# Optimization experiments

Measured on AMD Instinct MI355X. Metric: run time of the kernel, lower is better.

The kernel has to match this reference:

```python
import jax, jax.numpy as jnp
import numpy as np

FORGET_RADIX = 10
HIDDEN_RADIX = 23
LN2 = float(np.log(2.0))
MAX_FORGET = 0.875
BATCH, IN_SIZE, H_SIZE = 8192, 1024, 2048
G = H_SIZE // 2  # group size (h_size // 2)


def setup_inputs() -> dict:
    key = jax.random.key(0)
    ks = jax.random.split(key, 6)
    x = jax.random.normal(ks[0], (BATCH, IN_SIZE), dtype=jnp.float32)
    # hidden is a fixed-point (radix 23) int state; values correspond to floats in (-0.125, 0.125)
    hidden = jax.random.randint(ks[1], (BATCH, H_SIZE), -(2**20), 2**20, dtype=jnp.int32)

    def lin(k, fan_in, fan_out):
        kw, kb = jax.random.split(k)
        s = 1.0 / np.sqrt(fan_in)
        W = jax.random.uniform(kw, (fan_in, fan_out), jnp.float32, -s, s)
        b = jax.random.uniform(kb, (fan_out,), jnp.float32, -s, s)
        return W, b

    W_zr1, b_zr1 = lin(ks[2], IN_SIZE + G, H_SIZE)
    W_g1, b_g1 = lin(ks[3], IN_SIZE + G, G)
    W_zr2, b_zr2 = lin(ks[4], IN_SIZE + G, H_SIZE)
    W_g2, b_g2 = lin(ks[5], IN_SIZE + G, G)
    return {"x": x, "hidden": hidden,
            "W_zr1": W_zr1, "b_zr1": b_zr1, "W_g1": W_g1, "b_g1": b_g1,
            "W_zr2": W_zr2, "b_zr2": b_zr2, "W_g2": W_g2, "b_g2": b_g2,
            "slice_dim": 0}


def _to_float(h_fix, radix):
    # ConvertToFloat: fixed-point int -> float
    return h_fix.astype(jnp.float32) / np.float32(2.0 ** radix)


def _to_fixed(v, radix):
    # ConvertToFixed: float -> fixed-point int (truncation toward zero, like Tensor.int())
    return jnp.trunc(v * np.float32(2.0 ** radix)).astype(jnp.int64)


def reference(x, hidden, W_zr1, b_zr1, W_g1, b_g1, W_zr2, b_zr2, W_g2, b_g2, slice_dim):
    h = hidden.astype(jnp.int64)  # widen so h * z_fix (up to ~2^34) does not overflow
    h1, h2 = h[:, :G], h[:, G:]

    # ---- group 1 update (reads h2) ----
    h2_fl = _to_float(h2, HIDDEN_RADIX)
    zr1 = jax.nn.sigmoid(jnp.concatenate([x, h2_fl], axis=1) @ W_zr1 + b_zr1)
    z1, r1 = zr1[:, :G], zr1[:, G:]
    z1 = MAX_FORGET * z1 + (1.0 - MAX_FORGET)
    g1 = jnp.tanh(jnp.concatenate([x, r1 * h2_fl], axis=1) @ W_g1 + b_g1)
    z1_fix = jnp.maximum(_to_fixed(z1, FORGET_RADIX), 1)  # EnsureNotForgetAll
    h1 = jnp.floor_divide(h1 * z1_fix, 2 ** FORGET_RADIX)  # FixedMultiply, buf=None, mask=1
    h1 = h1 + _to_fixed((1.0 - z1) * g1, HIDDEN_RADIX)     # + MaskFixedMultiply(update1, 1)

    # ---- group 2 update (reads updated h1) ----
    h1_fl = _to_float(h1, HIDDEN_RADIX)
    zr2 = jax.nn.sigmoid(jnp.concatenate([x, h1_fl], axis=1) @ W_zr2 + b_zr2)
    z2, r2 = zr2[:, :G], zr2[:, G:]
    z2 = MAX_FORGET * z2 + (1.0 - MAX_FORGET)
    g2 = jnp.tanh(jnp.concatenate([x, r2 * h1_fl], axis=1) @ W_g2 + b_g2)
    z2_fix = jnp.maximum(_to_fixed(z2, FORGET_RADIX), 1)
    h2 = jnp.floor_divide(h2 * z2_fix, 2 ** FORGET_RADIX)
    h2 = h2 + _to_fixed((1.0 - z2) * g2, HIDDEN_RADIX)

    recurrent_hidden = jnp.concatenate([h1, h2], axis=1).astype(jnp.int32)
    output_hidden = recurrent_hidden.astype(jnp.float32) / np.float32(2.0 ** HIDDEN_RADIX)

    optimal_bits = (jnp.sum(-jnp.log(z1[:, slice_dim:]) / LN2)
                    + jnp.sum(-jnp.log(z2) / LN2)
                    + 32.0 * slice_dim * x.shape[0])
    return recurrent_hidden, output_hidden, optimal_bits
```

## Files before the change

### kernel.cpp

```cpp
#include <hip/hip_runtime.h>
#include <hip/hip_bf16.h>

#define BATCH   8192
#define IN_SZ   1024
#define HSZ     2048
#define GG      1024
#define KTOT    2048

typedef __hip_bfloat16 bf16;
typedef __attribute__((ext_vector_type(8))) short  short8;
typedef __attribute__((ext_vector_type(4))) float  floatx4;

typedef __attribute__((address_space(1))) const void gvoid_t;
typedef __attribute__((address_space(3))) void       lvoid_t;

__device__ __forceinline__ void async_ld16(void* lds, const void* g) {
  __builtin_amdgcn_global_load_lds((gvoid_t*)g, (lvoid_t*)lds, 16, 0, 0);
}

__global__ void prep_kernel(const float* __restrict__ x, bf16* __restrict__ xb,
                            const int* __restrict__ hidden, bf16* __restrict__ hf,
                            float* accp) {
  int idx = blockIdx.x * blockDim.x + threadIdx.x;
  int i = idx * 4;
  float4 xv = *(const float4*)(x + i);
  xb[i + 0] = __float2bfloat16(xv.x);
  xb[i + 1] = __float2bfloat16(xv.y);
  xb[i + 2] = __float2bfloat16(xv.z);
  xb[i + 3] = __float2bfloat16(xv.w);
  int m = i >> 10, j = i & 1023;
  int4 hv = *(const int4*)(hidden + m * HSZ + GG + j);
  const float sc = 1.0f / 8388608.0f;
  hf[i + 0] = __float2bfloat16((float)hv.x * sc);
  hf[i + 1] = __float2bfloat16((float)hv.y * sc);
  hf[i + 2] = __float2bfloat16((float)hv.z * sc);
  hf[i + 3] = __float2bfloat16((float)hv.w * sc);
  if (idx == 0) *accp = 0.0f;
}

__global__ void transpose_cast(const float* __restrict__ W, bf16* __restrict__ Wt,
                               int K, int N) {
  __shared__ float tile[32][33];
  int bx = blockIdx.x, by = blockIdx.y;
  int tx = threadIdx.x, ty = threadIdx.y;
  int n_in = bx * 32 + tx;
  int k_in = by * 32 + ty;
#pragma unroll
  for (int s = 0; s < 32; s += 8)
    tile[ty + s][tx] = W[(size_t)(k_in + s) * N + n_in];
  __syncthreads();
  int n_out = bx * 32 + ty;
  int k_out = by * 32 + tx;
#pragma unroll
  for (int s = 0; s < 32; s += 8)
    Wt[(size_t)(n_out + s) * K + k_out] = __float2bfloat16(tile[tx][ty + s]);
}

__device__ __forceinline__ void gemm_mainloop(const bf16* __restrict__ Aleft,
                                              const bf16* __restrict__ Aright,
                                              const bf16* __restrict__ Bt,
                                              bf16* As, bf16* Bs,
                                              int m0, int n0, floatx4 acc[4][4]) {
  int t = threadIdx.x;
  int r = t >> 2, c = t & 3;
  int lane = t & 63;
  int q = lane >> 4, r16 = lane & 15;
  int w = t >> 6;
  int wm = w & 1, wn = w >> 1;

  const size_t arow0 = (size_t)(m0 + r) * IN_SZ;
  const size_t arow1 = (size_t)(m0 + r + 64) * IN_SZ;
  const size_t brow0 = (size_t)(n0 + r) * KTOT;
  const size_t brow1 = (size_t)(n0 + r + 64) * KTOT;
  bf16* lA0 = As + t * 8;
  bf16* lA1 = As + 64 * 32 + t * 8;
  bf16* lB0 = Bs + t * 8;
  bf16* lB1 = Bs + 64 * 32 + t * 8;
  const bf16* aRd = As + (wm * 64 + r16) * 32 + q * 8;
  const bf16* bRd = Bs + (wn * 64 + r16) * 32 + q * 8;

  for (int kb = 0; kb < KTOT / 32; ++kb) {
    int kt = kb * 32;
    const bf16* asrc; int kloc;
    if (kt < IN_SZ) { asrc = Aleft;  kloc = kt; }
    else            { asrc = Aright; kloc = kt - IN_SZ; }
    int ac = kloc + c * 8;
    async_ld16(lA0, asrc + arow0 + ac);
    async_ld16(lA1, asrc + arow1 + ac);
    int bc = kt + c * 8;
    async_ld16(lB0, Bt + brow0 + bc);
    async_ld16(lB1, Bt + brow1 + bc);
    __syncthreads();
    short8 af[4], bfr[4];
#pragma unroll
    for (int i = 0; i < 4; ++i) af[i]  = *(const short8*)(const void*)(aRd + i * 16 * 32);
#pragma unroll
    for (int j = 0; j < 4; ++j) bfr[j] = *(const short8*)(const void*)(bRd + j * 16 * 32);
#pragma unroll
    for (int i = 0; i < 4; ++i)
#pragma unroll
      for (int j = 0; j < 4; ++j)
        acc[i][j] = __builtin_amdgcn_mfma_f32_16x16x32_bf16(af[i], bfr[j], acc[i][j], 0, 0, 0);
    __syncthreads();
  }
}

__global__ void gemm_zr(const bf16* __restrict__ xb, const bf16* __restrict__ hfp,
                        const bf16* __restrict__ Bt, const float* __restrict__ bias,
                        float* __restrict__ zbuf, bf16* __restrict__ rh,
                        const int* __restrict__ slice_ptr, int use_slice,
                        float* __restrict__ accp) {
  __shared__ bf16 As[128 * 32];
  __shared__ bf16 Bs[128 * 32];
  floatx4 acc[4][4];
#pragma unroll
  for (int i = 0; i < 4; ++i)
#pragma unroll
    for (int j = 0; j < 4; ++j) acc[i][j] = (floatx4)0.0f;

  int m0 = blockIdx.y * 128, n0 = blockIdx.x * 128;
  gemm_mainloop(xb, hfp, Bt, As, Bs, m0, n0, acc);

  int t = threadIdx.x;
  int lane = t & 63, q = lane >> 4, r16 = lane & 15;
  int w = t >> 6, wm = w & 1, wn = w >> 1;
  int nmin = use_slice ? *slice_ptr : 0;
  float lsum = 0.0f;

#pragma unroll
  for (int i = 0; i < 4; ++i) {
    int mbase = m0 + wm * 64 + i * 16 + q * 4;
#pragma unroll
    for (int j = 0; j < 4; ++j) {
      int n = n0 + wn * 64 + j * 16 + r16;
      float bn = bias[n];
#pragma unroll
      for (int rr = 0; rr < 4; ++rr) {
        int m = mbase + rr;
        float v = acc[i][j][rr] + bn;
        float s = 1.0f / (1.0f + __expf(-v));
        if (n < GG) {
          float z = 0.875f * s + 0.125f;
          zbuf[(size_t)m * GG + n] = z;
          if (n >= nmin) lsum += -__log2f(z);
        } else {
          int jc = n - GG;
          float hfl = __bfloat162float(hfp[(size_t)m * GG + jc]);
          rh[(size_t)m * GG + jc] = __float2bfloat16(s * hfl);
        }
      }
    }
  }
  __syncthreads();
  float* sf = (float*)As;
#pragma unroll
  for (int off = 32; off > 0; off >>= 1) lsum += __shfl_down(lsum, off, 64);
  if (lane == 0) sf[w] = lsum;
  __syncthreads();
  if (t == 0) atomicAdd(accp, sf[0] + sf[1] + sf[2] + sf[3]);
}

__global__ void gemm_g(const bf16* __restrict__ xb, const bf16* __restrict__ rh,
                       const bf16* __restrict__ Bt, const float* __restrict__ bias,
                       const float* __restrict__ zbuf, const int* __restrict__ hidden,
                       int col_off,
                       float* __restrict__ out0, float* __restrict__ out1,
                       bf16* __restrict__ hf_out, int write_hf,
                       int write_bits, const float* __restrict__ accp,
                       const int* __restrict__ slice_ptr, float* __restrict__ out2) {
  __shared__ bf16 As[128 * 32];
  __shared__ bf16 Bs[128 * 32];
  floatx4 acc[4][4];
#pragma unroll
  for (int i = 0; i < 4; ++i)
#pragma unroll
    for (int j = 0; j < 4; ++j) acc[i][j] = (floatx4)0.0f;

  int m0 = blockIdx.y * 128, n0 = blockIdx.x * 128;
  gemm_mainloop(xb, rh, Bt, As, Bs, m0, n0, acc);

  int t = threadIdx.x;
  int lane = t & 63, q = lane >> 4, r16 = lane & 15;
  int w = t >> 6, wm = w & 1, wn = w >> 1;

#pragma unroll
  for (int i = 0; i < 4; ++i) {
    int mbase = m0 + wm * 64 + i * 16 + q * 4;
#pragma unroll
    for (int j = 0; j < 4; ++j) {
      int n = n0 + wn * 64 + j * 16 + r16;
      float bn = bias[n];
#pragma unroll
      for (int rr = 0; rr < 4; ++rr) {
        int m = mbase + rr;
        float v = acc[i][j][rr] + bn;
        float e = __expf(2.0f * v);
        float g = 1.0f - 2.0f / (e + 1.0f);
        float z = zbuf[(size_t)m * GG + n];
        int zfix = (int)(z * 1024.0f);
        if (zfix < 1) zfix = 1;
        long long h = hidden[(size_t)m * HSZ + col_off + n];
        long long hupd = (h * (long long)zfix) >> 10;
        float t2 = (1.0f - z) * g * 8388608.0f;
        long long f2 = (long long)t2;
        int hnew = (int)(hupd + f2);
        size_t oidx = (size_t)m * HSZ + col_off + n;
        out0[oidx] = (float)hnew;
        float ofl = (float)hnew * (1.0f / 8388608.0f);
        out1[oidx] = ofl;
        if (write_hf) hf_out[(size_t)m * GG + n] = __float2bfloat16(ofl);
      }
    }
  }
  if (write_bits && blockIdx.x == 0 && blockIdx.y == 0 && t == 0) {
    *out2 = *accp + 32.0f * (float)(*slice_ptr) * (float)BATCH;
  }
}

extern "C" void kernel_launch(void* const* d_in, const int* in_sizes, int n_in,
                              void* d_out, int out_size, void* d_ws, size_t ws_size,
                              hipStream_t stream) {
  const float* x      = (const float*)d_in[0];
  const int*   hidden = (const int*)d_in[1];
  const float* W_zr1  = (const float*)d_in[2];
  const float* b_zr1  = (const float*)d_in[3];
  const float* W_g1   = (const float*)d_in[4];
  const float* b_g1   = (const float*)d_in[5];
  const float* W_zr2  = (const float*)d_in[6];
  const float* b_zr2  = (const float*)d_in[7];
  const float* W_g2   = (const float*)d_in[8];
  const float* b_g2   = (const float*)d_in[9];
  const int*   slice  = (const int*)d_in[10];

  char* ws = (char*)d_ws;
  size_t off = 0;
  auto alloc = [&](size_t bytes) -> void* {
    void* p = ws + off;
    off += (bytes + 255) & ~(size_t)255;
    return p;
  };
  bf16* xb     = (bf16*)alloc((size_t)BATCH * IN_SZ * 2);
  bf16* wt_zr1 = (bf16*)alloc((size_t)2048 * 2048 * 2);
  bf16* wt_g1  = (bf16*)alloc((size_t)1024 * 2048 * 2);
  bf16* wt_zr2 = (bf16*)alloc((size_t)2048 * 2048 * 2);
  bf16* wt_g2  = (bf16*)alloc((size_t)1024 * 2048 * 2);
  bf16* hf     = (bf16*)alloc((size_t)BATCH * GG * 2);
  bf16* rh     = (bf16*)alloc((size_t)BATCH * GG * 2);
  float* zbuf  = (float*)alloc((size_t)BATCH * GG * 4);
  float* accp  = (float*)alloc(256);

  float* out0 = (float*)d_out;
  float* out1 = out0 + (size_t)BATCH * HSZ;
  float* out2 = out0 + 2 * (size_t)BATCH * HSZ;

  prep_kernel<<<BATCH * IN_SZ / 4 / 256, 256, 0, stream>>>(x, xb, hidden, hf, accp);
  transpose_cast<<<dim3(64, 64), dim3(32, 8), 0, stream>>>(W_zr1, wt_zr1, 2048, 2048);
  transpose_cast<<<dim3(32, 64), dim3(32, 8), 0, stream>>>(W_g1,  wt_g1,  2048, 1024);
  transpose_cast<<<dim3(64, 64), dim3(32, 8), 0, stream>>>(W_zr2, wt_zr2, 2048, 2048);
  transpose_cast<<<dim3(32, 64), dim3(32, 8), 0, stream>>>(W_g2,  wt_g2,  2048, 1024);

  gemm_zr<<<dim3(16, 64), 256, 0, stream>>>(xb, hf, wt_zr1, b_zr1, zbuf, rh, slice, 1, accp);
  gemm_g<<<dim3(8, 64), 256, 0, stream>>>(xb, rh, wt_g1, b_g1, zbuf, hidden, 0,
                                          out0, out1, hf, 1, 0, accp, slice, out2);
  gemm_zr<<<dim3(16, 64), 256, 0, stream>>>(xb, hf, wt_zr2, b_zr2, zbuf, rh, slice, 0, accp);
  gemm_g<<<dim3(8, 64), 256, 0, stream>>>(xb, rh, wt_g2, b_g2, zbuf, hidden, 1024,
                                          out0, out1, hf, 0, 1, accp, slice, out2);
}
```

Before: 658.6 us.

## Swizzle LDS tiles, halve gemm_g M-tile, store z as bf16, fuse prep kernels

Merges the input casting and four weight transposes into one launch, using a vectorized 64x64 transpose tile. XOR-swizzles the LDS chunk placement to reduce bank conflicts on MFMA operand reads. Halves the M tile of the gate GEMM to double its block count for better CU fill, and stores the forget gate buffer as bf16 to cut its memory traffic. The bf16 z buffer can shift the fixed-point forget value by a few units, which risks output mismatches.

```diff
diff --git a/kernel.cpp b/kernel.cpp
--- a/kernel.cpp
+++ b/kernel.cpp
@@ -18,55 +18,75 @@
   __builtin_amdgcn_global_load_lds((gvoid_t*)g, (lvoid_t*)lds, 16, 0, 0);
 }
 
-__global__ void prep_kernel(const float* __restrict__ x, bf16* __restrict__ xb,
-                            const int* __restrict__ hidden, bf16* __restrict__ hf,
-                            float* accp) {
-  int idx = blockIdx.x * blockDim.x + threadIdx.x;
-  int i = idx * 4;
-  float4 xv = *(const float4*)(x + i);
-  xb[i + 0] = __float2bfloat16(xv.x);
-  xb[i + 1] = __float2bfloat16(xv.y);
-  xb[i + 2] = __float2bfloat16(xv.z);
-  xb[i + 3] = __float2bfloat16(xv.w);
-  int m = i >> 10, j = i & 1023;
-  int4 hv = *(const int4*)(hidden + m * HSZ + GG + j);
-  const float sc = 1.0f / 8388608.0f;
-  hf[i + 0] = __float2bfloat16((float)hv.x * sc);
-  hf[i + 1] = __float2bfloat16((float)hv.y * sc);
-  hf[i + 2] = __float2bfloat16((float)hv.z * sc);
-  hf[i + 3] = __float2bfloat16((float)hv.w * sc);
-  if (idx == 0) *accp = 0.0f;
-}
-
-__global__ void transpose_cast(const float* __restrict__ W, bf16* __restrict__ Wt,
-                               int K, int N) {
-  __shared__ float tile[32][33];
-  int bx = blockIdx.x, by = blockIdx.y;
-  int tx = threadIdx.x, ty = threadIdx.y;
-  int n_in = bx * 32 + tx;
-  int k_in = by * 32 + ty;
-#pragma unroll
-  for (int s = 0; s < 32; s += 8)
-    tile[ty + s][tx] = W[(size_t)(k_in + s) * N + n_in];
-  __syncthreads();
-  int n_out = bx * 32 + ty;
-  int k_out = by * 32 + tx;
-#pragma unroll
-  for (int s = 0; s < 32; s += 8)
-    Wt[(size_t)(n_out + s) * K + k_out] = __float2bfloat16(tile[tx][ty + s]);
-}
-
+__global__ void prep_all(const float* __restrict__ x, bf16* __restrict__ xb,
+                         const int* __restrict__ hidden, bf16* __restrict__ hf,
+                         float* accp,
+                         const float* __restrict__ W_zr1, const float* __restrict__ W_g1,
+                         const float* __restrict__ W_zr2, const float* __restrict__ W_g2,
+                         bf16* __restrict__ wt_zr1, bf16* __restrict__ wt_g1,
+                         bf16* __restrict__ wt_zr2, bf16* __restrict__ wt_g2) {
+  int b = blockIdx.x;
+  int t = threadIdx.x;
+  if (b < 3072) {
+    const float* W; bf16* Wt; int N; int tb = b;
+    if (tb < 1024)      { W = W_zr1; Wt = wt_zr1; N = 2048; }
+    else if (tb < 1536) { W = W_g1;  Wt = wt_g1;  N = 1024; tb -= 1024; }
+    else if (tb < 2560) { W = W_zr2; Wt = wt_zr2; N = 2048; tb -= 1536; }
+    else                { W = W_g2;  Wt = wt_g2;  N = 1024; tb -= 2560; }
+    int ntn = N >> 6;
+    int k0 = (tb / ntn) * 64, n0 = (tb % ntn) * 64;
+    __shared__ float tile[64][65];
+    int kk = t >> 4, nn = (t & 15) * 4;
+#pragma unroll
+    for (int s = 0; s < 4; ++s) {
+      int row = kk + s * 16;
+      float4 v = *(const float4*)&W[(size_t)(k0 + row) * N + n0 + nn];
+      tile[row][nn + 0] = v.x; tile[row][nn + 1] = v.y;
+      tile[row][nn + 2] = v.z; tile[row][nn + 3] = v.w;
+    }
+    __syncthreads();
+    int k8 = (t & 7) * 8;
+#pragma unroll
+    for (int s = 0; s < 2; ++s) {
+      int nl = (t >> 3) + s * 32;
+      bf16 vals[8];
+#pragma unroll
+      for (int u = 0; u < 8; ++u) vals[u] = __float2bfloat16(tile[k8 + u][nl]);
+      *(short8*)&Wt[(size_t)(n0 + nl) * KTOT + k0 + k8] = *(short8*)vals;
+    }
+  } else {
+    int idx = (b - 3072) * 256 + t;
+    int i = idx * 4;
+    float4 xv = *(const float4*)(x + i);
+    xb[i + 0] = __float2bfloat16(xv.x);
+    xb[i + 1] = __float2bfloat16(xv.y);
+    xb[i + 2] = __float2bfloat16(xv.z);
+    xb[i + 3] = __float2bfloat16(xv.w);
+    int m = i >> 10, j = i & 1023;
+    int4 hv = *(const int4*)(hidden + m * HSZ + GG + j);
+    const float sc = 1.0f / 8388608.0f;
+    hf[i + 0] = __float2bfloat16((float)hv.x * sc);
+    hf[i + 1] = __float2bfloat16((float)hv.y * sc);
+    hf[i + 2] = __float2bfloat16((float)hv.z * sc);
+    hf[i + 3] = __float2bfloat16((float)hv.w * sc);
+    if (idx == 0) *accp = 0.0f;
+  }
+}
+
+template<int BM, int MI>
 __device__ __forceinline__ void gemm_mainloop(const bf16* __restrict__ Aleft,
                                               const bf16* __restrict__ Aright,
                                               const bf16* __restrict__ Bt,
                                               bf16* As, bf16* Bs,
-                                              int m0, int n0, floatx4 acc[4][4]) {
-  int t = threadIdx.x;
-  int r = t >> 2, c = t & 3;
+                                              int m0, int n0, floatx4 (&acc)[MI][4]) {
+  int t = threadIdx.x;
+  int r = t >> 2;
+  int c2 = (t & 3) ^ ((t >> 3) & 3);
   int lane = t & 63;
   int q = lane >> 4, r16 = lane & 15;
   int w = t >> 6;
   int wm = w & 1, wn = w >> 1;
+  int swz = q ^ ((r16 >> 1) & 3);
 
   const size_t arow0 = (size_t)(m0 + r) * IN_SZ;
   const size_t arow1 = (size_t)(m0 + r + 64) * IN_SZ;
@@ -76,28 +96,28 @@
   bf16* lA1 = As + 64 * 32 + t * 8;
   bf16* lB0 = Bs + t * 8;
   bf16* lB1 = Bs + 64 * 32 + t * 8;
-  const bf16* aRd = As + (wm * 64 + r16) * 32 + q * 8;
-  const bf16* bRd = Bs + (wn * 64 + r16) * 32 + q * 8;
+  const bf16* aRd = As + (wm * (BM / 2) + r16) * 32 + swz * 8;
+  const bf16* bRd = Bs + (wn * 64 + r16) * 32 + swz * 8;
 
   for (int kb = 0; kb < KTOT / 32; ++kb) {
     int kt = kb * 32;
     const bf16* asrc; int kloc;
     if (kt < IN_SZ) { asrc = Aleft;  kloc = kt; }
     else            { asrc = Aright; kloc = kt - IN_SZ; }
-    int ac = kloc + c * 8;
+    int ac = kloc + c2 * 8;
     async_ld16(lA0, asrc + arow0 + ac);
-    async_ld16(lA1, asrc + arow1 + ac);
-    int bc = kt + c * 8;
+    if (BM == 128) async_ld16(lA1, asrc + arow1 + ac);
+    int bc = kt + c2 * 8;
     async_ld16(lB0, Bt + brow0 + bc);
     async_ld16(lB1, Bt + brow1 + bc);
     __syncthreads();
-    short8 af[4], bfr[4];
-#pragma unroll
-    for (int i = 0; i < 4; ++i) af[i]  = *(const short8*)(const void*)(aRd + i * 16 * 32);
-#pragma unroll
-    for (int j = 0; j < 4; ++j) bfr[j] = *(const short8*)(const void*)(bRd + j * 16 * 32);
-#pragma unroll
-    for (int i = 0; i < 4; ++i)
+    short8 af[MI], bfr[4];
+#pragma unroll
+    for (int i = 0; i < MI; ++i) af[i]  = *(const short8*)(const void*)(aRd + i * 16 * 32);
+#pragma unroll
+    for (int j = 0; j < 4; ++j)  bfr[j] = *(const short8*)(const void*)(bRd + j * 16 * 32);
+#pragma unroll
+    for (int i = 0; i < MI; ++i)
 #pragma unroll
       for (int j = 0; j < 4; ++j)
         acc[i][j] = __builtin_amdgcn_mfma_f32_16x16x32_bf16(af[i], bfr[j], acc[i][j], 0, 0, 0);
@@ -107,7 +127,7 @@
 
 __global__ void gemm_zr(const bf16* __restrict__ xb, const bf16* __restrict__ hfp,
                         const bf16* __restrict__ Bt, const float* __restrict__ bias,
-                        float* __restrict__ zbuf, bf16* __restrict__ rh,
+                        bf16* __restrict__ zbuf, bf16* __restrict__ rh,
                         const int* __restrict__ slice_ptr, int use_slice,
                         float* __restrict__ accp) {
   __shared__ bf16 As[128 * 32];
@@ -119,7 +139,7 @@
     for (int j = 0; j < 4; ++j) acc[i][j] = (floatx4)0.0f;
 
   int m0 = blockIdx.y * 128, n0 = blockIdx.x * 128;
-  gemm_mainloop(xb, hfp, Bt, As, Bs, m0, n0, acc);
+  gemm_mainloop<128, 4>(xb, hfp, Bt, As, Bs, m0, n0, acc);
 
   int t = threadIdx.x;
   int lane = t & 63, q = lane >> 4, r16 = lane & 15;
@@ -141,7 +161,7 @@
         float s = 1.0f / (1.0f + __expf(-v));
         if (n < GG) {
           float z = 0.875f * s + 0.125f;
-          zbuf[(size_t)m * GG + n] = z;
+          zbuf[(size_t)m * GG + n] = __float2bfloat16(z);
           if (n >= nmin) lsum += -__log2f(z);
         } else {
           int jc = n - GG;
@@ -162,30 +182,30 @@
 
 __global__ void gemm_g(const bf16* __restrict__ xb, const bf16* __restrict__ rh,
                        const bf16* __restrict__ Bt, const float* __restrict__ bias,
-                       const float* __restrict__ zbuf, const int* __restrict__ hidden,
+                       const bf16* __restrict__ zbuf, const int* __restrict__ hidden,
                        int col_off,
                        float* __restrict__ out0, float* __restrict__ out1,
                        bf16* __restrict__ hf_out, int write_hf,
                        int write_bits, const float* __restrict__ accp,
                        const int* __restrict__ slice_ptr, float* __restrict__ out2) {
-  __shared__ bf16 As[128 * 32];
+  __shared__ bf16 As[64 * 32];
   __shared__ bf16 Bs[128 * 32];
-  floatx4 acc[4][4];
-#pragma unroll
-  for (int i = 0; i < 4; ++i)
+  floatx4 acc[2][4];
+#pragma unroll
+  for (int i = 0; i < 2; ++i)
 #pragma unroll
     for (int j = 0; j < 4; ++j) acc[i][j] = (floatx4)0.0f;
 
-  int m0 = blockIdx.y * 128, n0 = blockIdx.x * 128;
-  gemm_mainloop(xb, rh, Bt, As, Bs, m0, n0, acc);
+  int m0 = blockIdx.y * 64, n0 = blockIdx.x * 128;
+  gemm_mainloop<64, 2>(xb, rh, Bt, As, Bs, m0, n0, acc);
 
   int t = threadIdx.x;
   int lane = t & 63, q = lane >> 4, r16 = lane & 15;
   int w = t >> 6, wm = w & 1, wn = w >> 1;
 
 #pragma unroll
-  for (int i = 0; i < 4; ++i) {
-    int mbase = m0 + wm * 64 + i * 16 + q * 4;
+  for (int i = 0; i < 2; ++i) {
+    int mbase = m0 + wm * 32 + i * 16 + q * 4;
 #pragma unroll
     for (int j = 0; j < 4; ++j) {
       int n = n0 + wn * 64 + j * 16 + r16;
@@ -196,7 +216,7 @@
         float v = acc[i][j][rr] + bn;
         float e = __expf(2.0f * v);
         float g = 1.0f - 2.0f / (e + 1.0f);
-        float z = zbuf[(size_t)m * GG + n];
+        float z = __bfloat162float(zbuf[(size_t)m * GG + n]);
         int zfix = (int)(z * 1024.0f);
         if (zfix < 1) zfix = 1;
         long long h = hidden[(size_t)m * HSZ + col_off + n];
@@ -246,23 +266,21 @@
   bf16* wt_g2  = (bf16*)alloc((size_t)1024 * 2048 * 2);
   bf16* hf     = (bf16*)alloc((size_t)BATCH * GG * 2);
   bf16* rh     = (bf16*)alloc((size_t)BATCH * GG * 2);
-  float* zbuf  = (float*)alloc((size_t)BATCH * GG * 4);
+  bf16* zbuf   = (bf16*)alloc((size_t)BATCH * GG * 2);
   float* accp  = (float*)alloc(256);
 
   float* out0 = (float*)d_out;
   float* out1 = out0 + (size_t)BATCH * HSZ;
   float* out2 = out0 + 2 * (size_t)BATCH * HSZ;
 
-  prep_kernel<<<BATCH * IN_SZ / 4 / 256, 256, 0, stream>>>(x, xb, hidden, hf, accp);
-  transpose_cast<<<dim3(64, 64), dim3(32, 8), 0, stream>>>(W_zr1, wt_zr1, 2048, 2048);
-  transpose_cast<<<dim3(32, 64), dim3(32, 8), 0, stream>>>(W_g1,  wt_g1,  2048, 1024);
-  transpose_cast<<<dim3(64, 64), dim3(32, 8), 0, stream>>>(W_zr2, wt_zr2, 2048, 2048);
-  transpose_cast<<<dim3(32, 64), dim3(32, 8), 0, stream>>>(W_g2,  wt_g2,  2048, 1024);
+  prep_all<<<3072 + 8192, 256, 0, stream>>>(x, xb, hidden, hf, accp,
+                                            W_zr1, W_g1, W_zr2, W_g2,
+                                            wt_zr1, wt_g1, wt_zr2, wt_g2);
 
   gemm_zr<<<dim3(16, 64), 256, 0, stream>>>(xb, hf, wt_zr1, b_zr1, zbuf, rh, slice, 1, accp);
-  gemm_g<<<dim3(8, 64), 256, 0, stream>>>(xb, rh, wt_g1, b_g1, zbuf, hidden, 0,
-                                          out0, out1, hf, 1, 0, accp, slice, out2);
+  gemm_g<<<dim3(8, 128), 256, 0, stream>>>(xb, rh, wt_g1, b_g1, zbuf, hidden, 0,
+                                           out0, out1, hf, 1, 0, accp, slice, out2);
   gemm_zr<<<dim3(16, 64), 256, 0, stream>>>(xb, hf, wt_zr2, b_zr2, zbuf, rh, slice, 0, accp);
-  gemm_g<<<dim3(8, 64), 256, 0, stream>>>(xb, rh, wt_g2, b_g2, zbuf, hidden, 1024,
-                                          out0, out1, hf, 0, 1, accp, slice, out2);
-}
+  gemm_g<<<dim3(8, 128), 256, 0, stream>>>(xb, rh, wt_g2, b_g2, zbuf, hidden, 1024,
+                                           out0, out1, hf, 0, 1, accp, slice, out2);
+}
```

After: 644.3 us. 1.02x faster.
